# Kernel optimization log

Measured on AMD Instinct MI355X. Metric: run time of the kernel, lower is better.

## Reference

```python
import jax, jax.numpy as jnp
import numpy as np

N0, N1, N2 = 200000, 600000, 400000
NNZ1, NNZ2 = 1200000, 1200000
G = 256          # number of graphs in the batch
H = 128          # num_hidden
NIN = 32         # num_input
L = 2            # num_layers
R = 3            # max_rank + 1


def setup_inputs() -> dict:
    key = jax.random.key(0)
    ks = jax.random.split(key, 24)
    d = {}
    d["x0"] = jax.random.normal(ks[0], (N0, NIN), jnp.float32)
    d["x1"] = jax.random.normal(ks[1], (N1, NIN), jnp.float32)
    d["x2"] = jax.random.normal(ks[2], (N2, NIN), jnp.float32)
    d["b1_rows"] = jax.random.randint(ks[3], (NNZ1,), 0, N0, jnp.int32)
    d["b1_cols"] = jax.random.randint(ks[4], (NNZ1,), 0, N1, jnp.int32)
    d["b2_rows"] = jax.random.randint(ks[5], (NNZ2,), 0, N1, jnp.int32)
    d["b2_cols"] = jax.random.randint(ks[6], (NNZ2,), 0, N2, jnp.int32)
    d["batch0"] = jnp.sort(jax.random.randint(ks[7], (N0,), 0, G, jnp.int32))
    d["batch1"] = jnp.sort(jax.random.randint(ks[8], (N1,), 0, G, jnp.int32))
    d["batch2"] = jnp.sort(jax.random.randint(ks[9], (N2,), 0, G, jnp.int32))
    sin = 1.0 / np.sqrt(NIN).astype(np.float32)
    sh = 1.0 / np.sqrt(H).astype(np.float32)
    d["w_emb"] = jax.random.normal(ks[10], (NIN, H), jnp.float32) * sin
    d["b_emb"] = jnp.zeros((H,), jnp.float32)
    # one conv weight per (layer, rank>0): message W for B_r^T @ (x @ W)
    d["conv_w"] = jax.random.normal(ks[11], (L, 2, H, H), jnp.float32) * sh
    d["pre_w1"] = jax.random.normal(ks[12], (R, H, H), jnp.float32) * sh
    d["pre_b1"] = jnp.zeros((R, H), jnp.float32)
    d["pre_w2"] = jax.random.normal(ks[13], (R, H, H), jnp.float32) * sh
    d["pre_b2"] = jnp.zeros((R, H), jnp.float32)
    d["post_w1"] = jax.random.normal(ks[14], (R * H, H), jnp.float32) * (1.0 / np.sqrt(R * H).astype(np.float32))
    d["post_b1"] = jnp.zeros((H,), jnp.float32)
    d["post_w2"] = jax.random.normal(ks[15], (H, 1), jnp.float32) * sh
    d["post_b2"] = jnp.zeros((1,), jnp.float32)
    return d


def reference(x0, x1, x2, b1_rows, b1_cols, b2_rows, b2_cols,
              batch0, batch1, batch2,
              w_emb, b_emb, conv_w,
              pre_w1, pre_b1, pre_w2, pre_b2,
              post_w1, post_b1, post_w2, post_b2):
    # feature embedding (shared across ranks)
    h0 = x0 @ w_emb + b_emb
    h1 = x1 @ w_emb + b_emb
    h2 = x2 @ w_emb + b_emb

    for l in range(L):
        # sparse incidence matmul B_r^T @ h_{r-1}: gather rows, scatter-add to cols
        m1 = jax.ops.segment_sum(h0[b1_rows], b1_cols, num_segments=N1)
        m2 = jax.ops.segment_sum(h1[b2_rows], b2_cols, num_segments=N2)
        # aggregation with sigmoid update; rank 0 has no incoming messages
        h0 = jax.nn.sigmoid(h0)
        h1 = jax.nn.sigmoid(m1 @ conv_w[l, 0])
        h2 = jax.nn.sigmoid(m2 @ conv_w[l, 1])

    def pre_pool(h, r):
        z = jax.nn.silu(h @ pre_w1[r] + pre_b1[r])
        return z @ pre_w2[r] + pre_b2[r]

    # global_add_pool per rank -> [G, H] each
    p0 = jax.ops.segment_sum(pre_pool(h0, 0), batch0, num_segments=G)
    p1 = jax.ops.segment_sum(pre_pool(h1, 1), batch1, num_segments=G)
    p2 = jax.ops.segment_sum(pre_pool(h2, 2), batch2, num_segments=G)

    state = jnp.concatenate([p0, p1, p2], axis=1)  # [G, 3H]
    z = jax.nn.silu(state @ post_w1 + post_b1)
    out = z @ post_w2 + post_b2                     # [G, 1]
    return jnp.squeeze(out, axis=-1)                # [G]
```

## Files before the change

### kernel.cpp

```cpp
#include <hip/hip_runtime.h>
#include <math.h>

#define HDIM 128
#define NIN_ 32
#define RANKS 3

typedef unsigned int u32;
typedef unsigned short u16;
typedef __attribute__((ext_vector_type(8))) short short8;
typedef __attribute__((ext_vector_type(8))) __bf16 bf16x8;
typedef __attribute__((ext_vector_type(4))) float f32x4;

__device__ __forceinline__ float bf2f(u16 b) { return __uint_as_float(((u32)b) << 16); }
__device__ __forceinline__ u16 f2bf(float f) {
    u32 u = __float_as_uint(f);
    u32 r = u + 0x7fffu + ((u >> 16) & 1u);
    return (u16)(r >> 16);
}
__device__ __forceinline__ float sigmoidf_(float x) {
    return __builtin_amdgcn_rcpf(1.0f + __builtin_amdgcn_exp2f(-1.44269504f * x));
}
__device__ __forceinline__ float siluf_(float x) { return x * sigmoidf_(x); }

template <int SIG>
__device__ __forceinline__ float sigpow(float f) {
#pragma unroll
    for (int q = 0; q < SIG; ++q) f = sigmoidf_(f);
    return f;
}

__global__ void zero_kernel(u32* __restrict__ p, long long nw) {
    long long i = (long long)blockIdx.x * blockDim.x + threadIdx.x;
    long long stride = (long long)gridDim.x * blockDim.x;
    for (; i < nw; i += stride) p[i] = 0u;
}

__global__ void count2_kernel(const int* __restrict__ c1, int n1, int* __restrict__ cntA,
                              const int* __restrict__ c2, int n2, int* __restrict__ cntB) {
    int e = blockIdx.x * 256 + threadIdx.x;
    if (e < n1) atomicAdd(&cntA[c1[e]], 1);
    else if (e < n1 + n2) atomicAdd(&cntB[c2[e - n1]], 1);
}

__global__ void fill2_kernel(const int* __restrict__ r1, const int* __restrict__ c1,
                             int* __restrict__ curA, int* __restrict__ esrc1, int n1,
                             const int* __restrict__ r2, const int* __restrict__ c2,
                             int* __restrict__ curB, int* __restrict__ esrc2, int n2) {
    int e = blockIdx.x * 256 + threadIdx.x;
    if (e < n1) {
        int i = atomicAdd(&curA[c1[e]], 1);
        esrc1[i] = r1[e];
    } else if (e < n1 + n2) {
        int ee = e - n1;
        int i = atomicAdd(&curB[c2[ee]], 1);
        esrc2[i] = r2[ee];
    }
}

__global__ void scan1_kernel(const int* __restrict__ cnt, int* __restrict__ bsum, int ndst) {
    __shared__ int lds[256];
    int base = blockIdx.x * 1024, t = threadIdx.x;
    int s = 0;
#pragma unroll
    for (int j = 0; j < 4; ++j) {
        int i = base + t * 4 + j;
        s += (i < ndst) ? cnt[i] : 0;
    }
    lds[t] = s;
    __syncthreads();
    for (int off = 128; off > 0; off >>= 1) {
        if (t < off) lds[t] += lds[t + off];
        __syncthreads();
    }
    if (t == 0) bsum[blockIdx.x] = lds[0];
}

__global__ void scan2_kernel(int* __restrict__ bsum, int nb, int* __restrict__ total) {
    __shared__ int lds[256];
    int t = threadIdx.x;
    int v[8];
    int s = 0;
#pragma unroll
    for (int j = 0; j < 8; ++j) {
        int i = t * 8 + j;
        v[j] = (i < nb) ? bsum[i] : 0;
        s += v[j];
    }
    lds[t] = s;
    __syncthreads();
    for (int off = 1; off < 256; off <<= 1) {
        int y = (t >= off) ? lds[t - off] : 0;
        __syncthreads();
        lds[t] += y;
        __syncthreads();
    }
    int run = lds[t] - s;
#pragma unroll
    for (int j = 0; j < 8; ++j) {
        int i = t * 8 + j;
        if (i < nb) {
            bsum[i] = run;
            run += v[j];
        }
    }
    if (t == 255) *total = run;
}

__global__ void scan3_kernel(const int* __restrict__ cnt, const int* __restrict__ bsum,
                             int* __restrict__ rowptr, int* __restrict__ cursor, int ndst) {
    __shared__ int lds[256];
    int base = blockIdx.x * 1024, t = threadIdx.x;
    int v[4];
    int s = 0;
#pragma unroll
    for (int j = 0; j < 4; ++j) {
        int i = base + t * 4 + j;
        v[j] = (i < ndst) ? cnt[i] : 0;
        s += v[j];
    }
    lds[t] = s;
    __syncthreads();
    for (int off = 1; off < 256; off <<= 1) {
        int y = (t >= off) ? lds[t - off] : 0;
        __syncthreads();
        lds[t] += y;
        __syncthreads();
    }
    int run = bsum[blockIdx.x] + lds[t] - s;
#pragma unroll
    for (int j = 0; j < 4; ++j) {
        int i = base + t * 4 + j;
        if (i < ndst) {
            rowptr[i] = run;
            cursor[i] = run;
            run += v[j];
        }
    }
}

__global__ void wprep_kernel(const float* __restrict__ conv_w, const float* __restrict__ pre_w1,
                             const float* __restrict__ pre_w2, u16* __restrict__ wt, int Lnum) {
    int tid = blockIdx.x * 256 + threadIdx.x;
    int nm = 2 * Lnum + 6;
    if (tid >= nm * 128 * 128) return;
    int m = tid >> 14;
    int r = tid & 16383;
    int k = r >> 7;
    int col = r & 127;
    const float* src;
    if (m < 2 * Lnum) src = conv_w + (size_t)m * 16384;
    else if (m < 2 * Lnum + 3) src = pre_w1 + (size_t)(m - 2 * Lnum) * 16384;
    else src = pre_w2 + (size_t)(m - 2 * Lnum - 3) * 16384;
    float v = src[k * 128 + col];
    wt[(size_t)m * 16384 + col * 128 + (k ^ ((col & 7) << 3))] = f2bf(v);
}

__global__ void wembprep_kernel(const float* __restrict__ w_emb, u16* __restrict__ wembT) {
    int tid = blockIdx.x * 256 + threadIdx.x;
    if (tid >= HDIM * NIN_) return;
    int col = tid >> 5, k = tid & 31;
    wembT[col * 32 + k] = f2bf(w_emb[k * HDIM + col]);
}

__global__ __launch_bounds__(512) void embed_mfma_kernel(const float* __restrict__ x,
                                                         const u16* __restrict__ wembT,
                                                         const float* __restrict__ b,
                                                         u16* __restrict__ h,
                                                         u16* __restrict__ hs, int n) {
    __shared__ u16 cs[8][16][128];
    const int tid = threadIdx.x;
    const int wave = tid >> 6, lane = tid & 63;
    const int row0 = blockIdx.x * 128;
    const int col = lane & 15, kg = lane >> 4;
    const int wrow0 = row0 + wave * 16;
    const int arow = wrow0 + col;
    const int arowc = arow < n ? arow : (n - 1);

    bf16x8 afrag;
    {
        const float4* xp = (const float4*)(x + (size_t)arowc * NIN_ + kg * 8);
        float4 xa = xp[0], xb = xp[1];
        short8 s;
        s[0] = (short)f2bf(xa.x); s[1] = (short)f2bf(xa.y);
        s[2] = (short)f2bf(xa.z); s[3] = (short)f2bf(xa.w);
        s[4] = (short)f2bf(xb.x); s[5] = (short)f2bf(xb.y);
        s[6] = (short)f2bf(xb.z); s[7] = (short)f2bf(xb.w);
        afrag = __builtin_bit_cast(bf16x8, s);
    }

    f32x4 accs[8];
#pragma unroll
    for (int ct = 0; ct < 8; ++ct) {
        int bcol = ct * 16 + col;
        bf16x8 bfrag = *(const bf16x8*)(wembT + bcol * 32 + kg * 8);
        f32x4 acc = (f32x4){0.f, 0.f, 0.f, 0.f};
        acc = __builtin_amdgcn_mfma_f32_16x16x32_bf16(afrag, bfrag, acc, 0, 0, 0);
        float bv = b[bcol];
#pragma unroll
        for (int r = 0; r < 4; ++r) acc[r] += bv;
        accs[ct] = acc;
#pragma unroll
        for (int r = 0; r < 4; ++r) {
            int crow = kg * 4 + r;
            cs[wave][crow][(ct * 16 + col) ^ ((crow & 7) << 3)] = f2bf(acc[r]);
        }
    }
#pragma unroll
    for (int it = 0; it < 4; ++it) {
        int cid = it * 64 + lane;
        int r = cid >> 4, c = cid & 15;
        int grow = wrow0 + r;
        if (grow < n) {
            short8 v = *(const short8*)(&cs[wave][r][(c * 8) ^ ((r & 7) << 3)]);
            *(short8*)(h + (size_t)grow * HDIM + c * 8) = v;
        }
    }
    if (hs) {
#pragma unroll
        for (int ct = 0; ct < 8; ++ct)
#pragma unroll
            for (int r = 0; r < 4; ++r) {
                int crow = kg * 4 + r;
                cs[wave][crow][(ct * 16 + col) ^ ((crow & 7) << 3)] = f2bf(sigmoidf_(accs[ct][r]));
            }
#pragma unroll
        for (int it = 0; it < 4; ++it) {
            int cid = it * 64 + lane;
            int r = cid >> 4, c = cid & 15;
            int grow = wrow0 + r;
            if (grow < n) {
                short8 v = *(const short8*)(&cs[wave][r][(c * 8) ^ ((r & 7) << 3)]);
                *(short8*)(hs + (size_t)grow * HDIM + c * 8) = v;
            }
        }
    }
}

__device__ __forceinline__ void gemm128(const bf16x8 afrag[4], const u16* wls, f32x4 acc[8],
                                        int col, int kg) {
#pragma unroll
    for (int ct = 0; ct < 8; ++ct) {
        int bcol = ct * 16 + col;
        const u16* bb = wls + bcol * 128;
        int swz = (bcol & 7) << 3;
#pragma unroll
        for (int k0 = 0; k0 < 4; ++k0) {
            bf16x8 bfrag = *(const bf16x8*)(bb + ((k0 * 32 + kg * 8) ^ swz));
            acc[ct] = __builtin_amdgcn_mfma_f32_16x16x32_bf16(afrag[k0], bfrag, acc[ct], 0, 0, 0);
        }
    }
}

__device__ __forceinline__ void stage_w(const u16* __restrict__ w, u16* wls, int tid) {
    const uint4* g = (const uint4*)w;
    uint4* l = (uint4*)wls;
#pragma unroll
    for (int i = 0; i < 4; ++i) l[tid + i * 512] = g[tid + i * 512];
}

__device__ __forceinline__ void pool_acc(const f32x4 acc[8], const float* __restrict__ b2,
                                         const int* __restrict__ batch, float* __restrict__ p,
                                         int n, int colOff, int wrow0, int col, int kg) {
    if (wrow0 >= n) return;
    int rend = wrow0 + 15 < n ? wrow0 + 15 : (n - 1);
    int bstart = batch[wrow0];
    int bend = batch[rend];
    if (bstart == bend) {
#pragma unroll
        for (int ct = 0; ct < 8; ++ct) {
            float b2v = b2[ct * 16 + col];
            float s = 0.f;
#pragma unroll
            for (int r = 0; r < 4; ++r) {
                int row = wrow0 + kg * 4 + r;
                if (row < n) s += acc[ct][r] + b2v;
            }
            s += __shfl_xor(s, 16, 64);
            s += __shfl_xor(s, 32, 64);
            if (kg == 0) atomicAdd(&p[bstart * (RANKS * HDIM) + colOff + ct * 16 + col], s);
        }
    } else {
        int bgs[4];
#pragma unroll
        for (int r = 0; r < 4; ++r) {
            int row = wrow0 + kg * 4 + r;
            bgs[r] = (row < n) ? batch[row] : -1;
        }
#pragma unroll
        for (int ct = 0; ct < 8; ++ct) {
            float b2v = b2[ct * 16 + col];
            int curb = -1;
            float cur = 0.f;
#pragma unroll
            for (int r = 0; r < 4; ++r) {
                if (bgs[r] >= 0) {
                    if (bgs[r] != curb) {
                        if (curb >= 0)
                            atomicAdd(&p[curb * (RANKS * HDIM) + colOff + ct * 16 + col], cur);
                        curb = bgs[r];
                        cur = 0.f;
                    }
                    cur += acc[ct][r] + b2v;
                }
            }
            if (curb >= 0) atomicAdd(&p[curb * (RANKS * HDIM) + colOff + ct * 16 + col], cur);
        }
    }
}

template <int SIGA>
__global__ __launch_bounds__(512) void merged_n1_kernel(
    const u16* __restrict__ srcA, const u16* __restrict__ srcS,
    const int* __restrict__ rowptr, const int* __restrict__ esrc,
    const u16* __restrict__ wc0, const u16* __restrict__ wc1,
    const u16* __restrict__ w1t, const u16* __restrict__ w2t,
    const float* __restrict__ b1, const float* __restrict__ b2,
    const int* __restrict__ batch, float* __restrict__ p, int colOff,
    u16* __restrict__ outB, int n) {
    __shared__ u16 wls[16384];
    __shared__ u16 zs[8][16][128];
    const int tid = threadIdx.x;
    const int wave = tid >> 6, lane = tid & 63;
    const int row0 = blockIdx.x * 128;
    const int col = lane & 15, kg = lane >> 4;
    const int wrow0 = row0 + wave * 16;

    stage_w(wc0, wls, tid);

    float gr[4][8], gs[4][8];
#pragma unroll
    for (int k0 = 0; k0 < 4; ++k0)
#pragma unroll
        for (int j = 0; j < 8; ++j) { gr[k0][j] = 0.f; gs[k0][j] = 0.f; }

    const int arow = wrow0 + col;
    if (arow < n) {
        int beg = rowptr[arow], end = rowptr[arow + 1];
        if constexpr (SIGA == 0) {
            for (int e = beg; e < end; e += 2) {
                int s0 = esrc[e];
                bool has1 = (e + 1 < end);
                int s1 = has1 ? esrc[e + 1] : s0;
                const bf16x8* pa0 = (const bf16x8*)(srcA + (size_t)s0 * HDIM + kg * 8);
                const bf16x8* ps0 = (const bf16x8*)(srcS + (size_t)s0 * HDIM + kg * 8);
                const bf16x8* pa1 = (const bf16x8*)(srcA + (size_t)s1 * HDIM + kg * 8);
                const bf16x8* ps1 = (const bf16x8*)(srcS + (size_t)s1 * HDIM + kg * 8);
                bf16x8 va0[4], vs0[4], va1[4], vs1[4];
#pragma unroll
                for (int k0 = 0; k0 < 4; ++k0) {
                    va0[k0] = pa0[k0 * 4]; vs0[k0] = ps0[k0 * 4];
                    va1[k0] = pa1[k0 * 4]; vs1[k0] = ps1[k0 * 4];
                }
#pragma unroll
                for (int k0 = 0; k0 < 4; ++k0) {
                    short8 a = __builtin_bit_cast(short8, va0[k0]);
                    short8 s = __builtin_bit_cast(short8, vs0[k0]);
#pragma unroll
                    for (int j = 0; j < 8; ++j) {
                        gr[k0][j] += bf2f((u16)a[j]);
                        gs[k0][j] += bf2f((u16)s[j]);
                    }
                }
                if (has1) {
#pragma unroll
                    for (int k0 = 0; k0 < 4; ++k0) {
                        short8 a = __builtin_bit_cast(short8, va1[k0]);
                        short8 s = __builtin_bit_cast(short8, vs1[k0]);
#pragma unroll
                        for (int j = 0; j < 8; ++j) {
                            gr[k0][j] += bf2f((u16)a[j]);
                            gs[k0][j] += bf2f((u16)s[j]);
                        }
                    }
                }
            }
        } else {
            for (int e = beg; e < end; e += 2) {
                int s0 = esrc[e];
                bool has1 = (e + 1 < end);
                int s1 = has1 ? esrc[e + 1] : s0;
                const bf16x8* p0 = (const bf16x8*)(srcA + (size_t)s0 * HDIM + kg * 8);
                const bf16x8* p1 = (const bf16x8*)(srcA + (size_t)s1 * HDIM + kg * 8);
                bf16x8 v0[4], v1[4];
#pragma unroll
                for (int k0 = 0; k0 < 4; ++k0) { v0[k0] = p0[k0 * 4]; v1[k0] = p1[k0 * 4]; }
#pragma unroll
                for (int k0 = 0; k0 < 4; ++k0) {
                    short8 sv = __builtin_bit_cast(short8, v0[k0]);
#pragma unroll
                    for (int j = 0; j < 8; ++j) {
                        float f = sigpow<SIGA>(bf2f((u16)sv[j]));
                        gr[k0][j] += f;
                        gs[k0][j] += sigmoidf_(f);
                    }
                }
                if (has1) {
#pragma unroll
                    for (int k0 = 0; k0 < 4; ++k0) {
                        short8 sv = __builtin_bit_cast(short8, v1[k0]);
#pragma unroll
                        for (int j = 0; j < 8; ++j) {
                            float f = sigpow<SIGA>(bf2f((u16)sv[j]));
                            gr[k0][j] += f;
                            gs[k0][j] += sigmoidf_(f);
                        }
                    }
                }
            }
        }
    }
    bf16x8 afragR[4], afragS[4];
#pragma unroll
    for (int k0 = 0; k0 < 4; ++k0) {
        short8 sR, sS;
#pragma unroll
        for (int j = 0; j < 8; ++j) {
            sR[j] = (short)f2bf(gr[k0][j]);
            sS[j] = (short)f2bf(gs[k0][j]);
        }
        afragR[k0] = __builtin_bit_cast(bf16x8, sR);
        afragS[k0] = __builtin_bit_cast(bf16x8, sS);
    }
    __syncthreads();

    f32x4 acc[8];
#pragma unroll
    for (int ct = 0; ct < 8; ++ct) acc[ct] = (f32x4){0.f, 0.f, 0.f, 0.f};
    gemm128(afragR, wls, acc, col, kg);
#pragma unroll
    for (int ct = 0; ct < 8; ++ct)
#pragma unroll
        for (int r = 0; r < 4; ++r) {
            int crow = kg * 4 + r;
            zs[wave][crow][(ct * 16 + col) ^ ((crow & 7) << 3)] = f2bf(sigmoidf_(acc[ct][r]));
        }
#pragma unroll
    for (int it = 0; it < 4; ++it) {
        int cid = it * 64 + lane;
        int r = cid >> 4, c = cid & 15;
        int grow = wrow0 + r;
        if (grow < n) {
            short8 v = *(const short8*)(&zs[wave][r][(c * 8) ^ ((r & 7) << 3)]);
            __builtin_nontemporal_store(v, (short8*)(outB + (size_t)grow * HDIM + c * 8));
        }
    }

    __syncthreads();
    stage_w(wc1, wls, tid);
    __syncthreads();

#pragma unroll
    for (int ct = 0; ct < 8; ++ct) acc[ct] = (f32x4){0.f, 0.f, 0.f, 0.f};
    gemm128(afragS, wls, acc, col, kg);
#pragma unroll
    for (int ct = 0; ct < 8; ++ct)
#pragma unroll
        for (int r = 0; r < 4; ++r) {
            int crow = kg * 4 + r;
            zs[wave][crow][(ct * 16 + col) ^ ((crow & 7) << 3)] = f2bf(sigmoidf_(acc[ct][r]));
        }
    __syncthreads();
    stage_w(w1t, wls, tid);
    __syncthreads();

    bf16x8 zfrag[4];
    {
        int zswz = (col & 7) << 3;
#pragma unroll
        for (int k0 = 0; k0 < 4; ++k0)
            zfrag[k0] = *(const bf16x8*)(&zs[wave][col][(k0 * 32 + kg * 8) ^ zswz]);
    }
#pragma unroll
    for (int ct = 0; ct < 8; ++ct) acc[ct] = (f32x4){0.f, 0.f, 0.f, 0.f};
    gemm128(zfrag, wls, acc, col, kg);
#pragma unroll
    for (int ct = 0; ct < 8; ++ct) {
        float b1v = b1[ct * 16 + col];
#pragma unroll
        for (int r = 0; r < 4; ++r) {
            int crow = kg * 4 + r;
            zs[wave][crow][(ct * 16 + col) ^ ((crow & 7) << 3)] = f2bf(siluf_(acc[ct][r] + b1v));
        }
    }
    __syncthreads();
    stage_w(w2t, wls, tid);
    __syncthreads();

    {
        int zswz = (col & 7) << 3;
#pragma unroll
        for (int k0 = 0; k0 < 4; ++k0)
            zfrag[k0] = *(const bf16x8*)(&zs[wave][col][(k0 * 32 + kg * 8) ^ zswz]);
    }
#pragma unroll
    for (int ct = 0; ct < 8; ++ct) acc[ct] = (f32x4){0.f, 0.f, 0.f, 0.f};
    gemm128(zfrag, wls, acc, col, kg);

    pool_acc(acc, b2, batch, p, n, colOff, wrow0, col, kg);
}

template <int MODE, int SIG>
__global__ __launch_bounds__(512) void fused_mfma_kernel(
    const u16* __restrict__ srcbuf, const int* __restrict__ rowptr,
    const int* __restrict__ esrc, const u16* __restrict__ wconv,
    const u16* __restrict__ w1t, const u16* __restrict__ w2t,
    const float* __restrict__ b1, const float* __restrict__ b2,
    const int* __restrict__ batch, float* __restrict__ p, int colOff,
    u16* __restrict__ outB, int n) {
    __shared__ u16 wls[16384];
    __shared__ u16 zs[8][16][128];
    const int tid = threadIdx.x;
    const int wave = tid >> 6, lane = tid & 63;
    const int row0 = blockIdx.x * 128;
    const int col = lane & 15, kg = lane >> 4;
    const int wrow0 = row0 + wave * 16;

    stage_w(wconv, wls, tid);

    float ga[4][8];
#pragma unroll
    for (int k0 = 0; k0 < 4; ++k0)
#pragma unroll
        for (int j = 0; j < 8; ++j) ga[k0][j] = 0.f;
    const int arow = wrow0 + col;
    if (arow < n) {
        int beg = rowptr[arow], end = rowptr[arow + 1];
        for (int e = beg; e < end; e += 2) {
            int s0 = esrc[e];
            bool has1 = (e + 1 < end);
            int s1 = has1 ? esrc[e + 1] : s0;
            const bf16x8* p0 = (const bf16x8*)(srcbuf + (size_t)s0 * HDIM + kg * 8);
            const bf16x8* p1 = (const bf16x8*)(srcbuf + (size_t)s1 * HDIM + kg * 8);
            bf16x8 v0[4], v1[4];
#pragma unroll
            for (int k0 = 0; k0 < 4; ++k0) { v0[k0] = p0[k0 * 4]; v1[k0] = p1[k0 * 4]; }
#pragma unroll
            for (int k0 = 0; k0 < 4; ++k0) {
                short8 sv = __builtin_bit_cast(short8, v0[k0]);
#pragma unroll
                for (int j = 0; j < 8; ++j) ga[k0][j] += sigpow<SIG>(bf2f((u16)sv[j]));
            }
            if (has1) {
#pragma unroll
                for (int k0 = 0; k0 < 4; ++k0) {
                    short8 sv = __builtin_bit_cast(short8, v1[k0]);
#pragma unroll
                    for (int j = 0; j < 8; ++j) ga[k0][j] += sigpow<SIG>(bf2f((u16)sv[j]));
                }
            }
        }
    }
    bf16x8 afrag[4];
#pragma unroll
    for (int k0 = 0; k0 < 4; ++k0) {
        short8 s;
#pragma unroll
        for (int j = 0; j < 8; ++j) s[j] = (short)f2bf(ga[k0][j]);
        afrag[k0] = __builtin_bit_cast(bf16x8, s);
    }
    __syncthreads();

    f32x4 acc[8];
#pragma unroll
    for (int ct = 0; ct < 8; ++ct) acc[ct] = (f32x4){0.f, 0.f, 0.f, 0.f};
    gemm128(afrag, wls, acc, col, kg);

#pragma unroll
    for (int ct = 0; ct < 8; ++ct)
#pragma unroll
        for (int r = 0; r < 4; ++r) {
            int crow = kg * 4 + r;
            zs[wave][crow][(ct * 16 + col) ^ ((crow & 7) << 3)] = f2bf(sigmoidf_(acc[ct][r]));
        }

    if (MODE == 0) {
#pragma unroll
        for (int it = 0; it < 4; ++it) {
            int cid = it * 64 + lane;
            int r = cid >> 4, c = cid & 15;
            int grow = wrow0 + r;
            if (grow < n) {
                short8 v = *(const short8*)(&zs[wave][r][(c * 8) ^ ((r & 7) << 3)]);
                __builtin_nontemporal_store(v, (short8*)(outB + (size_t)grow * HDIM + c * 8));
            }
        }
        return;
    }

    __syncthreads();
    stage_w(w1t, wls, tid);
    __syncthreads();

    bf16x8 zfrag[4];
    {
        int zswz = (col & 7) << 3;
#pragma unroll
        for (int k0 = 0; k0 < 4; ++k0)
            zfrag[k0] = *(const bf16x8*)(&zs[wave][col][(k0 * 32 + kg * 8) ^ zswz]);
    }
#pragma unroll
    for (int ct = 0; ct < 8; ++ct) acc[ct] = (f32x4){0.f, 0.f, 0.f, 0.f};
    gemm128(zfrag, wls, acc, col, kg);
#pragma unroll
    for (int ct = 0; ct < 8; ++ct) {
        float b1v = b1[ct * 16 + col];
#pragma unroll
        for (int r = 0; r < 4; ++r) {
            int crow = kg * 4 + r;
            zs[wave][crow][(ct * 16 + col) ^ ((crow & 7) << 3)] = f2bf(siluf_(acc[ct][r] + b1v));
        }
    }
    __syncthreads();
    stage_w(w2t, wls, tid);
    __syncthreads();

    {
        int zswz = (col & 7) << 3;
#pragma unroll
        for (int k0 = 0; k0 < 4; ++k0)
            zfrag[k0] = *(const bf16x8*)(&zs[wave][col][(k0 * 32 + kg * 8) ^ zswz]);
    }
#pragma unroll
    for (int ct = 0; ct < 8; ++ct) acc[ct] = (f32x4){0.f, 0.f, 0.f, 0.f};
    gemm128(zfrag, wls, acc, col, kg);

    pool_acc(acc, b2, batch, p, n, colOff, wrow0, col, kg);
}

template <int SIG>
__global__ __launch_bounds__(512) void prepool_mfma_kernel(
    const u16* __restrict__ h, const u16* __restrict__ w1t, const u16* __restrict__ w2t,
    const float* __restrict__ b1, const float* __restrict__ b2, const int* __restrict__ batch,
    float* __restrict__ p, int n, int colOff) {
    __shared__ u16 wls[16384];
    __shared__ u16 zs[8][16][128];
    const int tid = threadIdx.x;
    const int wave = tid >> 6, lane = tid & 63;
    const int row0 = blockIdx.x * 128;
    const int col = lane & 15, kg = lane >> 4;
    const int wrow0 = row0 + wave * 16;

    stage_w(w1t, wls, tid);

    const int arow = wrow0 + col;
    const int arowc = arow < n ? arow : (n - 1);
    bf16x8 afrag[4];
    {
        const bf16x8* ap = (const bf16x8*)(h + (size_t)arowc * HDIM + kg * 8);
#pragma unroll
        for (int k0 = 0; k0 < 4; ++k0) afrag[k0] = ap[k0 * 4];
    }
    if (SIG > 0) {
#pragma unroll
        for (int k0 = 0; k0 < 4; ++k0) {
            short8 s = __builtin_bit_cast(short8, afrag[k0]);
#pragma unroll
            for (int j = 0; j < 8; ++j) s[j] = (short)f2bf(sigpow<SIG>(bf2f((u16)s[j])));
            afrag[k0] = __builtin_bit_cast(bf16x8, s);
        }
    }
    __syncthreads();

    f32x4 acc[8];
#pragma unroll
    for (int ct = 0; ct < 8; ++ct) acc[ct] = (f32x4){0.f, 0.f, 0.f, 0.f};
    gemm128(afrag, wls, acc, col, kg);
#pragma unroll
    for (int ct = 0; ct < 8; ++ct) {
        float b1v = b1[ct * 16 + col];
#pragma unroll
        for (int r = 0; r < 4; ++r) {
            int crow = kg * 4 + r;
            zs[wave][crow][(ct * 16 + col) ^ ((crow & 7) << 3)] = f2bf(siluf_(acc[ct][r] + b1v));
        }
    }
    __syncthreads();
    stage_w(w2t, wls, tid);
    __syncthreads();

    bf16x8 zfrag[4];
    {
        int zswz = (col & 7) << 3;
#pragma unroll
        for (int k0 = 0; k0 < 4; ++k0)
            zfrag[k0] = *(const bf16x8*)(&zs[wave][col][(k0 * 32 + kg * 8) ^ zswz]);
    }
#pragma unroll
    for (int ct = 0; ct < 8; ++ct) acc[ct] = (f32x4){0.f, 0.f, 0.f, 0.f};
    gemm128(zfrag, wls, acc, col, kg);

    pool_acc(acc, b2, batch, p, n, colOff, wrow0, col, kg);
}

__global__ void final_kernel(const float* __restrict__ p, const float* __restrict__ w1,
                             const float* __restrict__ b1, const float* __restrict__ w2,
                             const float* __restrict__ b2, float* __restrict__ out) {
    const int g = blockIdx.x;
    const int c = threadIdx.x;
    const float* pg = p + g * (RANKS * HDIM);
    float acc = b1[c];
    for (int k = 0; k < RANKS * HDIM; ++k) acc = fmaf(pg[k], w1[k * HDIM + c], acc);
    float z = siluf_(acc);
    float v = z * w2[c];
#pragma unroll
    for (int off = 32; off > 0; off >>= 1) v += __shfl_down(v, off, 64);
    __shared__ float red[2];
    if ((c & 63) == 0) red[c >> 6] = v;
    __syncthreads();
    if (c == 0) out[g] = red[0] + red[1] + b2[0];
}

extern "C" void kernel_launch(void* const* d_in, const int* in_sizes, int n_in,
                              void* d_out, int out_size, void* d_ws, size_t ws_size,
                              hipStream_t stream) {
    const float* x0 = (const float*)d_in[0];
    const float* x1 = (const float*)d_in[1];
    const int* b1_rows = (const int*)d_in[3];
    const int* b1_cols = (const int*)d_in[4];
    const int* b2_rows = (const int*)d_in[5];
    const int* b2_cols = (const int*)d_in[6];
    const int* batch0 = (const int*)d_in[7];
    const int* batch1 = (const int*)d_in[8];
    const int* batch2 = (const int*)d_in[9];
    const float* w_emb = (const float*)d_in[10];
    const float* b_emb = (const float*)d_in[11];
    const float* conv_w = (const float*)d_in[12];
    const float* pre_w1 = (const float*)d_in[13];
    const float* pre_b1 = (const float*)d_in[14];
    const float* pre_w2 = (const float*)d_in[15];
    const float* pre_b2 = (const float*)d_in[16];
    const float* post_w1 = (const float*)d_in[17];
    const float* post_b1 = (const float*)d_in[18];
    const float* post_w2 = (const float*)d_in[19];
    const float* post_b2 = (const float*)d_in[20];

    const int N0 = in_sizes[0] / NIN_;
    const int N1 = in_sizes[1] / NIN_;
    const int N2 = in_sizes[2] / NIN_;
    const int NNZ1 = in_sizes[3];
    const int NNZ2 = in_sizes[5];
    const int L = in_sizes[12] / (2 * HDIM * HDIM);
    const int Gn = out_size;

    u16* A = (u16*)d_ws;
    u16* As = A + (size_t)N0 * HDIM;
    u16* B = As + (size_t)N0 * HDIM;
    float* p = (float*)(B + (size_t)N1 * HDIM);
    u16* wt = (u16*)(p + (size_t)Gn * RANKS * HDIM);
    const u16* wt_conv = wt;
    const u16* wt_p1 = wt + (size_t)2 * L * 16384;
    const u16* wt_p2 = wt_p1 + (size_t)3 * 16384;
    u16* wembT = wt + (size_t)(2 * L + 6) * 16384;
    int* ip = (int*)(wembT + 4096);
    int* rowptr1 = ip;  ip += N1 + 1;
    int* rowptr2 = ip;  ip += N2 + 1;
    int* esrc1 = ip;    ip += NNZ1;
    int* esrc2 = ip;    ip += NNZ2;
    int* cntA = ip;     ip += N1;
    int* cntB = ip;     ip += N2;
    int* curA = ip;     ip += N1;
    int* curB = ip;     ip += N2;
    int* bsum = ip;     ip += 2048;

    {
        int tot = (2 * L + 6) * 16384;
        wprep_kernel<<<(tot + 255) / 256, 256, 0, stream>>>(conv_w, pre_w1, pre_w2, wt, L);
        wembprep_kernel<<<16, 256, 0, stream>>>(w_emb, wembT);

        zero_kernel<<<1024, 256, 0, stream>>>((u32*)cntA, (long long)(N1 + N2));
        count2_kernel<<<(NNZ1 + NNZ2 + 255) / 256, 256, 0, stream>>>(b1_cols, NNZ1, cntA,
                                                                     b2_cols, NNZ2, cntB);
        int nb1 = (N1 + 1023) / 1024;
        scan1_kernel<<<nb1, 256, 0, stream>>>(cntA, bsum, N1);
        scan2_kernel<<<1, 256, 0, stream>>>(bsum, nb1, rowptr1 + N1);
        scan3_kernel<<<nb1, 256, 0, stream>>>(cntA, bsum, rowptr1, curA, N1);
        int nb2 = (N2 + 1023) / 1024;
        scan1_kernel<<<nb2, 256, 0, stream>>>(cntB, bsum, N2);
        scan2_kernel<<<1, 256, 0, stream>>>(bsum, nb2, rowptr2 + N2);
        scan3_kernel<<<nb2, 256, 0, stream>>>(cntB, bsum, rowptr2, curB, N2);
        fill2_kernel<<<(NNZ1 + NNZ2 + 255) / 256, 256, 0, stream>>>(
            b1_rows, b1_cols, curA, esrc1, NNZ1, b2_rows, b2_cols, curB, esrc2, NNZ2);
    }

    embed_mfma_kernel<<<(N0 + 127) / 128, 512, 0, stream>>>(x0, wembT, b_emb, A, As, N0);

    zero_kernel<<<64, 256, 0, stream>>>((u32*)p, (long long)Gn * RANKS * HDIM);

    if (L >= 2) {
        int grid = (N1 + 127) / 128;
        const u16* wc0 = wt_conv + (size_t)((L - 2) * 2 + 0) * 16384;
        const u16* wc1 = wt_conv + (size_t)((L - 1) * 2 + 0) * 16384;
        switch (L - 2) {
            case 0: merged_n1_kernel<0><<<grid, 512, 0, stream>>>(
                        A, As, rowptr1, esrc1, wc0, wc1, wt_p1 + 16384, wt_p2 + 16384,
                        pre_b1 + HDIM, pre_b2 + HDIM, batch1, p, HDIM, B, N1); break;
            case 1: merged_n1_kernel<1><<<grid, 512, 0, stream>>>(
                        A, As, rowptr1, esrc1, wc0, wc1, wt_p1 + 16384, wt_p2 + 16384,
                        pre_b1 + HDIM, pre_b2 + HDIM, batch1, p, HDIM, B, N1); break;
            default: merged_n1_kernel<2><<<grid, 512, 0, stream>>>(
                        A, As, rowptr1, esrc1, wc0, wc1, wt_p1 + 16384, wt_p2 + 16384,
                        pre_b1 + HDIM, pre_b2 + HDIM, batch1, p, HDIM, B, N1); break;
        }
    } else {
        embed_mfma_kernel<<<(N1 + 127) / 128, 512, 0, stream>>>(x1, wembT, b_emb, B, nullptr, N1);
        fused_mfma_kernel<1, 0><<<(N1 + 127) / 128, 512, 0, stream>>>(
            A, rowptr1, esrc1, wt_conv, wt_p1 + 16384, wt_p2 + 16384,
            pre_b1 + HDIM, pre_b2 + HDIM, batch1, p, HDIM, nullptr, N1);
    }

    fused_mfma_kernel<1, 0><<<(N2 + 127) / 128, 512, 0, stream>>>(
        B, rowptr2, esrc2, wt_conv + (size_t)((L - 1) * 2 + 1) * 16384,
        wt_p1 + 2 * 16384, wt_p2 + 2 * 16384, pre_b1 + 2 * HDIM, pre_b2 + 2 * HDIM,
        batch2, p, 2 * HDIM, nullptr, N2);

    {
        int grid = (N0 + 127) / 128;
        switch (L - 1) {
            case 0: prepool_mfma_kernel<0><<<grid, 512, 0, stream>>>(
                        As, wt_p1, wt_p2, pre_b1, pre_b2, batch0, p, N0, 0); break;
            case 1: prepool_mfma_kernel<1><<<grid, 512, 0, stream>>>(
                        As, wt_p1, wt_p2, pre_b1, pre_b2, batch0, p, N0, 0); break;
            default: prepool_mfma_kernel<2><<<grid, 512, 0, stream>>>(
                        As, wt_p1, wt_p2, pre_b1, pre_b2, batch0, p, N0, 0); break;
        }
    }

    final_kernel<<<Gn, HDIM, 0, stream>>>(p, post_w1, post_b1, post_w2, post_b2, (float*)d_out);
}
```

Baseline: 783.4 us.

## Fuse rank-0 pre-pool MLP and pooling into the embedding kernel

The rank-0 pre-pool MLP and global add pool now run inside the embedding kernel, working on the sigmoid tile already held in shared memory. This removes the separate prepool launch and the re-read of the As buffer for N0 rows. The embedding kernel now needs extra shared memory for staged weights plus more block syncs, which may lower occupancy. Separately, the nontemporal stores of outB in the merged kernels become plain stores so the data can stay in cache for later reads.

After: 771.1 us. No clear change (-1.6%).

```diff
diff --git a/kernel.cpp b/kernel.cpp
--- a/kernel.cpp
+++ b/kernel.cpp
@@ -162,12 +162,87 @@
     wembT[col * 32 + k] = f2bf(w_emb[k * HDIM + col]);
 }
 
-__global__ __launch_bounds__(512) void embed_mfma_kernel(const float* __restrict__ x,
-                                                         const u16* __restrict__ wembT,
-                                                         const float* __restrict__ b,
-                                                         u16* __restrict__ h,
-                                                         u16* __restrict__ hs, int n) {
+__device__ __forceinline__ void gemm128(const bf16x8 afrag[4], const u16* wls, f32x4 acc[8],
+                                        int col, int kg) {
+#pragma unroll
+    for (int ct = 0; ct < 8; ++ct) {
+        int bcol = ct * 16 + col;
+        const u16* bb = wls + bcol * 128;
+        int swz = (bcol & 7) << 3;
+#pragma unroll
+        for (int k0 = 0; k0 < 4; ++k0) {
+            bf16x8 bfrag = *(const bf16x8*)(bb + ((k0 * 32 + kg * 8) ^ swz));
+            acc[ct] = __builtin_amdgcn_mfma_f32_16x16x32_bf16(afrag[k0], bfrag, acc[ct], 0, 0, 0);
+        }
+    }
+}
+
+__device__ __forceinline__ void stage_w(const u16* __restrict__ w, u16* wls, int tid) {
+    const uint4* g = (const uint4*)w;
+    uint4* l = (uint4*)wls;
+#pragma unroll
+    for (int i = 0; i < 4; ++i) l[tid + i * 512] = g[tid + i * 512];
+}
+
+__device__ __forceinline__ void pool_acc(const f32x4 acc[8], const float* __restrict__ b2,
+                                         const int* __restrict__ batch, float* __restrict__ p,
+                                         int n, int colOff, int wrow0, int col, int kg) {
+    if (wrow0 >= n) return;
+    int rend = wrow0 + 15 < n ? wrow0 + 15 : (n - 1);
+    int bstart = batch[wrow0];
+    int bend = batch[rend];
+    if (bstart == bend) {
+#pragma unroll
+        for (int ct = 0; ct < 8; ++ct) {
+            float b2v = b2[ct * 16 + col];
+            float s = 0.f;
+#pragma unroll
+            for (int r = 0; r < 4; ++r) {
+                int row = wrow0 + kg * 4 + r;
+                if (row < n) s += acc[ct][r] + b2v;
+            }
+            s += __shfl_xor(s, 16, 64);
+            s += __shfl_xor(s, 32, 64);
+            if (kg == 0) atomicAdd(&p[bstart * (RANKS * HDIM) + colOff + ct * 16 + col], s);
+        }
+    } else {
+        int bgs[4];
+#pragma unroll
+        for (int r = 0; r < 4; ++r) {
+            int row = wrow0 + kg * 4 + r;
+            bgs[r] = (row < n) ? batch[row] : -1;
+        }
+#pragma unroll
+        for (int ct = 0; ct < 8; ++ct) {
+            float b2v = b2[ct * 16 + col];
+            int curb = -1;
+            float cur = 0.f;
+#pragma unroll
+            for (int r = 0; r < 4; ++r) {
+                if (bgs[r] >= 0) {
+                    if (bgs[r] != curb) {
+                        if (curb >= 0)
+                            atomicAdd(&p[curb * (RANKS * HDIM) + colOff + ct * 16 + col], cur);
+                        curb = bgs[r];
+                        cur = 0.f;
+                    }
+                    cur += acc[ct][r] + b2v;
+                }
+            }
+            if (curb >= 0) atomicAdd(&p[curb * (RANKS * HDIM) + colOff + ct * 16 + col], cur);
+        }
+    }
+}
+
+template <int SIGP>
+__global__ __launch_bounds__(512) void embed_mfma_kernel(
+    const float* __restrict__ x, const u16* __restrict__ wembT, const float* __restrict__ b,
+    u16* __restrict__ h, u16* __restrict__ hs,
+    const u16* __restrict__ w1t, const u16* __restrict__ w2t,
+    const float* __restrict__ b1, const float* __restrict__ b2,
+    const int* __restrict__ batch, float* __restrict__ p, int colOff, int n) {
     __shared__ u16 cs[8][16][128];
+    __shared__ u16 wls[16384];
     const int tid = threadIdx.x;
     const int wave = tid >> 6, lane = tid & 63;
     const int row0 = blockIdx.x * 128;
@@ -175,6 +250,8 @@
     const int wrow0 = row0 + wave * 16;
     const int arow = wrow0 + col;
     const int arowc = arow < n ? arow : (n - 1);
+
+    if (SIGP >= 0) stage_w(w1t, wls, tid);
 
     bf16x8 afrag;
     {
@@ -234,77 +311,55 @@
             }
         }
     }
-}
-
-__device__ __forceinline__ void gemm128(const bf16x8 afrag[4], const u16* wls, f32x4 acc[8],
-                                        int col, int kg) {
-#pragma unroll
-    for (int ct = 0; ct < 8; ++ct) {
-        int bcol = ct * 16 + col;
-        const u16* bb = wls + bcol * 128;
-        int swz = (bcol & 7) << 3;
-#pragma unroll
-        for (int k0 = 0; k0 < 4; ++k0) {
-            bf16x8 bfrag = *(const bf16x8*)(bb + ((k0 * 32 + kg * 8) ^ swz));
-            acc[ct] = __builtin_amdgcn_mfma_f32_16x16x32_bf16(afrag[k0], bfrag, acc[ct], 0, 0, 0);
-        }
-    }
-}
-
-__device__ __forceinline__ void stage_w(const u16* __restrict__ w, u16* wls, int tid) {
-    const uint4* g = (const uint4*)w;
-    uint4* l = (uint4*)wls;
-#pragma unroll
-    for (int i = 0; i < 4; ++i) l[tid + i * 512] = g[tid + i * 512];
-}
-
-__device__ __forceinline__ void pool_acc(const f32x4 acc[8], const float* __restrict__ b2,
-                                         const int* __restrict__ batch, float* __restrict__ p,
-                                         int n, int colOff, int wrow0, int col, int kg) {
-    if (wrow0 >= n) return;
-    int rend = wrow0 + 15 < n ? wrow0 + 15 : (n - 1);
-    int bstart = batch[wrow0];
-    int bend = batch[rend];
-    if (bstart == bend) {
+
+    if constexpr (SIGP >= 0) {
+        bf16x8 afragP[4];
+        {
+            int zswz = (col & 7) << 3;
+#pragma unroll
+            for (int k0 = 0; k0 < 4; ++k0)
+                afragP[k0] = *(const bf16x8*)(&cs[wave][col][(k0 * 32 + kg * 8) ^ zswz]);
+        }
+        if (SIGP > 0) {
+#pragma unroll
+            for (int k0 = 0; k0 < 4; ++k0) {
+                short8 s = __builtin_bit_cast(short8, afragP[k0]);
+#pragma unroll
+                for (int j = 0; j < 8; ++j) s[j] = (short)f2bf(sigpow<SIGP>(bf2f((u16)s[j])));
+                afragP[k0] = __builtin_bit_cast(bf16x8, s);
+            }
+        }
+        __syncthreads();
+
+        f32x4 acc[8];
+#pragma unroll
+        for (int ct = 0; ct < 8; ++ct) acc[ct] = (f32x4){0.f, 0.f, 0.f, 0.f};
+        gemm128(afragP, wls, acc, col, kg);
 #pragma unroll
         for (int ct = 0; ct < 8; ++ct) {
-            float b2v = b2[ct * 16 + col];
-            float s = 0.f;
+            float b1v = b1[ct * 16 + col];
 #pragma unroll
             for (int r = 0; r < 4; ++r) {
-                int row = wrow0 + kg * 4 + r;
-                if (row < n) s += acc[ct][r] + b2v;
-            }
-            s += __shfl_xor(s, 16, 64);
-            s += __shfl_xor(s, 32, 64);
-            if (kg == 0) atomicAdd(&p[bstart * (RANKS * HDIM) + colOff + ct * 16 + col], s);
-        }
-    } else {
-        int bgs[4];
-#pragma unroll
-        for (int r = 0; r < 4; ++r) {
-            int row = wrow0 + kg * 4 + r;
-            bgs[r] = (row < n) ? batch[row] : -1;
-        }
-#pragma unroll
-        for (int ct = 0; ct < 8; ++ct) {
-            float b2v = b2[ct * 16 + col];
-            int curb = -1;
-            float cur = 0.f;
-#pragma unroll
-            for (int r = 0; r < 4; ++r) {
-                if (bgs[r] >= 0) {
-                    if (bgs[r] != curb) {
-                        if (curb >= 0)
-                            atomicAdd(&p[curb * (RANKS * HDIM) + colOff + ct * 16 + col], cur);
-                        curb = bgs[r];
-                        cur = 0.f;
-                    }
-                    cur += acc[ct][r] + b2v;
-                }
-            }
-            if (curb >= 0) atomicAdd(&p[curb * (RANKS * HDIM) + colOff + ct * 16 + col], cur);
-        }
+                int crow = kg * 4 + r;
+                cs[wave][crow][(ct * 16 + col) ^ ((crow & 7) << 3)] = f2bf(siluf_(acc[ct][r] + b1v));
+            }
+        }
+        __syncthreads();
+        stage_w(w2t, wls, tid);
+        __syncthreads();
+
+        bf16x8 zfrag[4];
+        {
+            int zswz = (col & 7) << 3;
+#pragma unroll
+            for (int k0 = 0; k0 < 4; ++k0)
+                zfrag[k0] = *(const bf16x8*)(&cs[wave][col][(k0 * 32 + kg * 8) ^ zswz]);
+        }
+#pragma unroll
+        for (int ct = 0; ct < 8; ++ct) acc[ct] = (f32x4){0.f, 0.f, 0.f, 0.f};
+        gemm128(zfrag, wls, acc, col, kg);
+
+        pool_acc(acc, b2, batch, p, n, colOff, wrow0, col, kg);
     }
 }
 
@@ -441,7 +496,7 @@
         int grow = wrow0 + r;
         if (grow < n) {
             short8 v = *(const short8*)(&zs[wave][r][(c * 8) ^ ((r & 7) << 3)]);
-            __builtin_nontemporal_store(v, (short8*)(outB + (size_t)grow * HDIM + c * 8));
+            *(short8*)(outB + (size_t)grow * HDIM + c * 8) = v;
         }
     }
 
@@ -581,7 +636,7 @@
             int grow = wrow0 + r;
             if (grow < n) {
                 short8 v = *(const short8*)(&zs[wave][r][(c * 8) ^ ((r & 7) << 3)]);
-                __builtin_nontemporal_store(v, (short8*)(outB + (size_t)grow * HDIM + c * 8));
+                *(short8*)(outB + (size_t)grow * HDIM + c * 8) = v;
             }
         }
         return;
@@ -782,9 +837,22 @@
             b1_rows, b1_cols, curA, esrc1, NNZ1, b2_rows, b2_cols, curB, esrc2, NNZ2);
     }
 
-    embed_mfma_kernel<<<(N0 + 127) / 128, 512, 0, stream>>>(x0, wembT, b_emb, A, As, N0);
-
     zero_kernel<<<64, 256, 0, stream>>>((u32*)p, (long long)Gn * RANKS * HDIM);
+
+    {
+        int grid = (N0 + 127) / 128;
+        if (L == 1) {
+            embed_mfma_kernel<0><<<grid, 512, 0, stream>>>(
+                x0, wembT, b_emb, A, As, wt_p1, wt_p2, pre_b1, pre_b2, batch0, p, 0, N0);
+        } else if (L == 2) {
+            embed_mfma_kernel<1><<<grid, 512, 0, stream>>>(
+                x0, wembT, b_emb, A, As, wt_p1, wt_p2, pre_b1, pre_b2, batch0, p, 0, N0);
+        } else {
+            embed_mfma_kernel<-1><<<grid, 512, 0, stream>>>(
+                x0, wembT, b_emb, A, As, nullptr, nullptr, nullptr, nullptr, nullptr, nullptr,
+                0, N0);
+        }
+    }
 
     if (L >= 2) {
         int grid = (N1 + 127) / 128;
@@ -802,7 +870,9 @@
                         pre_b1 + HDIM, pre_b2 + HDIM, batch1, p, HDIM, B, N1); break;
         }
     } else {
-        embed_mfma_kernel<<<(N1 + 127) / 128, 512, 0, stream>>>(x1, wembT, b_emb, B, nullptr, N1);
+        embed_mfma_kernel<-1><<<(N1 + 127) / 128, 512, 0, stream>>>(
+            x1, wembT, b_emb, B, nullptr, nullptr, nullptr, nullptr, nullptr, nullptr, nullptr,
+            0, N1);
         fused_mfma_kernel<1, 0><<<(N1 + 127) / 128, 512, 0, stream>>>(
             A, rowptr1, esrc1, wt_conv, wt_p1 + 16384, wt_p2 + 16384,
             pre_b1 + HDIM, pre_b2 + HDIM, batch1, p, HDIM, nullptr, N1);
@@ -813,16 +883,10 @@
         wt_p1 + 2 * 16384, wt_p2 + 2 * 16384, pre_b1 + 2 * HDIM, pre_b2 + 2 * HDIM,
         batch2, p, 2 * HDIM, nullptr, N2);
 
-    {
+    if (L >= 3) {
         int grid = (N0 + 127) / 128;
-        switch (L - 1) {
-            case 0: prepool_mfma_kernel<0><<<grid, 512, 0, stream>>>(
-                        As, wt_p1, wt_p2, pre_b1, pre_b2, batch0, p, N0, 0); break;
-            case 1: prepool_mfma_kernel<1><<<grid, 512, 0, stream>>>(
-                        As, wt_p1, wt_p2, pre_b1, pre_b2, batch0, p, N0, 0); break;
-            default: prepool_mfma_kernel<2><<<grid, 512, 0, stream>>>(
-                        As, wt_p1, wt_p2, pre_b1, pre_b2, batch0, p, N0, 0); break;
-        }
+        prepool_mfma_kernel<2><<<grid, 512, 0, stream>>>(
+            As, wt_p1, wt_p2, pre_b1, pre_b2, batch0, p, N0, 0);
     }
 
     final_kernel<<<Gn, HDIM, 0, stream>>>(p, post_w1, post_b1, post_w2, post_b2, (float*)d_out);
```
